# Kernel tuning notes

Hardware: AMD Instinct MI355X
Metric: run time of the kernel (lower is better)

## Reference

```python
import jax, jax.numpy as jnp
import numpy as np

N_NODES = 200000
N_EDGES = 6400000
F_OUT = 128
N_GRAPHS = 64


def setup_inputs() -> dict:
    key = jax.random.key(0)
    ks = jax.random.split(key, 6)
    x = jax.random.normal(ks[0], (N_NODES, 1), dtype=jnp.float32)
    edge_index = jax.random.randint(ks[1], (2, N_EDGES), 0, N_NODES, dtype=jnp.int64)
    batch = jnp.sort(jax.random.randint(ks[2], (N_NODES,), 0, N_GRAPHS, dtype=jnp.int64))
    edge_weights = jax.random.uniform(ks[3], (N_EDGES,), dtype=jnp.float32)
    W_l = jax.random.normal(ks[4], (F_OUT, 1), dtype=jnp.float32)
    b_l = jnp.zeros((F_OUT,), dtype=jnp.float32)
    W_r = jax.random.normal(ks[5], (F_OUT, 1), dtype=jnp.float32)
    return {"x": x, "edge_index": edge_index, "batch": batch,
            "edge_weights": edge_weights, "W_l": W_l, "b_l": b_l, "W_r": W_r}


def reference(x, edge_index, batch, edge_weights, W_l, b_l, W_r):
    # SAGEConv (mean aggregation, edge-weighted messages as in PyG propagate):
    #   out_i = lin_l( mean_{j in N(i)} w_ij * x_j ) + lin_r(x_i)
    n = x.shape[0]
    src, dst = edge_index[0], edge_index[1]
    msgs = x[src] * edge_weights[:, None]                      # [E, 1] gather
    agg_sum = jax.ops.segment_sum(msgs, dst, num_segments=n)  # [N, 1] scatter-add
    deg = jax.ops.segment_sum(jnp.ones((src.shape[0],), x.dtype), dst, num_segments=n)
    agg = agg_sum / jnp.maximum(deg, 1.0)[:, None]             # mean
    h = agg @ W_l.T + b_l + x @ W_r.T                          # [N, F_OUT]
    # dropout(p=0.2) is identity in eval mode -> omitted
    out = jax.ops.segment_max(h, batch, num_segments=N_GRAPHS)  # global_max_pool
    return out
```

## Files before the change

kernel.cpp:

```cpp
#include <hip/hip_runtime.h>
#include <hip/hip_bf16.h>
#include <float.h>
#include <math.h>

constexpr int NN = 200000;
constexpr int NE = 6400000;
constexpr int FO = 128;
constexpr int NG = 64;

constexpr int NCHUNK = 512;
constexpr int CHUNK  = NE / NCHUNK;
constexpr int C4     = CHUNK / 4;
constexpr int BNODES = 1024;
constexpr int NBUK   = (NN + BNODES - 1) / BNODES;

constexpr float Q_SCALE = 4096.0f;
constexpr float Q_INV   = 1.0f / 4096.0f;

__device__ __forceinline__ unsigned encf(float f) {
    unsigned u = __float_as_uint(f);
    return (u & 0x80000000u) ? ~u : (u | 0x80000000u);
}
__device__ __forceinline__ float decf(unsigned e) {
    unsigned u = (e & 0x80000000u) ? (e & 0x7FFFFFFFu) : ~e;
    return __uint_as_float(u);
}

__global__ __launch_bounds__(1024) void k_hist(const int* __restrict__ ei, unsigned* __restrict__ cnt,
                       unsigned* __restrict__ out_enc,
                       const int* __restrict__ batch, int* __restrict__ start) {
    __shared__ unsigned h[NBUK];
    int c = blockIdx.x, tid = threadIdx.x;
    for (int i = tid; i < NBUK; i += 1024) h[i] = 0u;
    if (c == 0) for (int i = tid; i < NG * FO; i += 1024) out_enc[i] = encf(-INFINITY);
    if (c == 1 && tid <= NG) {
        if (tid == NG) start[tid] = NN;
        else {
            int lo = 0, hi = NN;
            while (lo < hi) { int mid = (lo + hi) >> 1; if (batch[mid] < tid) lo = mid + 1; else hi = mid; }
            start[tid] = lo;
        }
    }
    __syncthreads();
    const int4* d4 = (const int4*)(ei + NE + c * CHUNK);
#pragma unroll
    for (int k = 0; k < 4; ++k) {
        int idx = tid + k * 1024;
        if (idx < C4) {
            int4 v = d4[idx];
            atomicAdd(&h[v.x >> 10], 1u);
            atomicAdd(&h[v.y >> 10], 1u);
            atomicAdd(&h[v.z >> 10], 1u);
            atomicAdd(&h[v.w >> 10], 1u);
        }
    }
    __syncthreads();
    for (int i = tid; i < NBUK; i += 1024) cnt[i * NCHUNK + c] = h[i];
}

__global__ void k_scanA(unsigned* __restrict__ cnt, unsigned* __restrict__ T) {
    __shared__ unsigned s[NCHUNK];
    int b = blockIdx.x, t = threadIdx.x;
    unsigned v = cnt[b * NCHUNK + t];
    s[t] = v;
    __syncthreads();
    for (int off = 1; off < NCHUNK; off <<= 1) {
        unsigned u = (t >= off) ? s[t - off] : 0u;
        __syncthreads();
        s[t] += u;
        __syncthreads();
    }
    cnt[b * NCHUNK + t] = s[t] - v;
    if (t == NCHUNK - 1) T[b] = s[t];
}

__global__ void k_scanB(const unsigned* __restrict__ T, unsigned* __restrict__ B) {
    __shared__ unsigned s[256];
    int t = threadIdx.x;
    unsigned v = (t < NBUK) ? T[t] : 0u;
    s[t] = v;
    __syncthreads();
    for (int off = 1; off < 256; off <<= 1) {
        unsigned u = (t >= off) ? s[t - off] : 0u;
        __syncthreads();
        s[t] += u;
        __syncthreads();
    }
    if (t < NBUK) B[t] = s[t] - v;
    if (t == 255) B[NBUK] = s[255];
}

__global__ __launch_bounds__(1024) void k_place(const int* __restrict__ ei, const float* __restrict__ x,
                        const float* __restrict__ w,
                        const unsigned* __restrict__ cnt,
                        const unsigned* __restrict__ T,
                        const unsigned* __restrict__ B,
                        unsigned* __restrict__ rec,
                        int blo, int bhi, unsigned cap) {
    __shared__ unsigned lincl[256];
    __shared__ unsigned loffs[NBUK];
    __shared__ unsigned gbase[NBUK];
    __shared__ unsigned recbuf[CHUNK];
    int c = blockIdx.x, tid = threadIdx.x;
    int nb = bhi - blo;

    unsigned sz = 0;
    if (tid < nb) {
        int b = blo + tid;
        unsigned pre = cnt[b * NCHUNK + c];
        unsigned nxt = (c + 1 < NCHUNK) ? cnt[b * NCHUNK + c + 1] : T[b];
        sz = nxt - pre;
        gbase[b] = B[b] - B[blo] + pre;
    }
    if (tid < 256) lincl[tid] = sz;
    __syncthreads();
    for (int off = 1; off < 256; off <<= 1) {
        unsigned v = 0;
        if (tid < 256 && tid >= off) v = lincl[tid - off];
        __syncthreads();
        if (tid < 256) lincl[tid] += v;
        __syncthreads();
    }
    if (tid < nb) loffs[blo + tid] = lincl[tid] - sz;
    __syncthreads();

    const int4*   s4 = (const int4*)(ei + c * CHUNK);
    const int4*   d4 = (const int4*)(ei + NE + c * CHUNK);
    const float4* w4 = (const float4*)(w + c * CHUNK);
#pragma unroll
    for (int k = 0; k < 4; ++k) {
        int idx = tid + k * 1024;
        if (idx >= C4) continue;
        int4   sv = s4[idx];
        int4   dv = d4[idx];
        float4 wv = w4[idx];
        int    ds[4] = {dv.x, dv.y, dv.z, dv.w};
        int    ss[4] = {sv.x, sv.y, sv.z, sv.w};
        float  wf[4] = {wv.x, wv.y, wv.z, wv.w};
#pragma unroll
        for (int j = 0; j < 4; ++j) {
            int d = ds[j], b = d >> 10;
            if (b < blo || b >= bhi) continue;
            float m = x[ss[j]] * wf[j];
            int q = __float2int_rn(m * Q_SCALE) + 32768;
            q = min(max(q, 0), 65535);
            unsigned lslot = atomicAdd(&loffs[b], 1u);
            recbuf[lslot] = ((unsigned)(d & (BNODES - 1)) << 16) | (unsigned)q;
        }
    }
    __syncthreads();

    int wave = tid >> 6, lane = tid & 63;
    for (int lb = wave; lb < nb; lb += 16) {
        unsigned s0 = lb ? lincl[lb - 1] : 0u;
        unsigned s1 = lincl[lb];
        unsigned g0 = gbase[blo + lb];
        for (unsigned i = s0 + lane; i < s1; i += 64) {
            unsigned g = g0 + (i - s0);
            if (g < cap) rec[g] = recbuf[i];
        }
    }
}

__global__ __launch_bounds__(1024) void k_bucket(const unsigned* __restrict__ rec,
                         const unsigned* __restrict__ B,
                         float* __restrict__ mean, int blo) {
    __shared__ unsigned long long acc[BNODES];
    int b = blo + blockIdx.x, tid = threadIdx.x;
    for (int i = tid; i < BNODES; i += 1024) acc[i] = 0ull;
    __syncthreads();
    unsigned b0 = B[blo];
    unsigned r0 = B[b] - b0, r1 = B[b + 1] - b0;
    for (unsigned r = r0 + tid; r < r1; r += 1024) {
        unsigned v = rec[r];
        atomicAdd(&acc[v >> 16], (1ull << 48) | (unsigned long long)(v & 0xFFFFu));
    }
    __syncthreads();
    int n0 = b * BNODES;
    for (int i = tid; i < BNODES; i += 1024) {
        int n = n0 + i;
        if (n < NN) {
            unsigned long long a = acc[i];
            float cn = (float)(unsigned)(a >> 48);
            float sq = (float)(a & 0xFFFFFFFFFFFFull);
            float sum = (sq - 32768.0f * cn) * Q_INV;
            mean[n] = sum / fmaxf(cn, 1.0f);
        }
    }
}

constexpr int SPLITS = 16;
__global__ void k_max8(const float* __restrict__ mean, const float* __restrict__ x,
                       const float* __restrict__ Wl, const float* __restrict__ Wr,
                       const int* __restrict__ start, unsigned* __restrict__ out_enc) {
    int g = blockIdx.x;
    int lo = start[g], hi = start[g + 1];
    int len = hi - lo;
    if (len <= 0) return;
    int per = (len + gridDim.y - 1) / gridDim.y;
    int a0 = lo + blockIdx.y * per;
    int a1 = min(a0 + per, hi);
    if (a0 >= a1) return;
    int f = threadIdx.x;
    float wl = Wl[f], wr = Wr[f];
    float m0 = -INFINITY, m1 = -INFINITY;
    int i = a0;
    for (; i + 2 <= a1; i += 2) {
        m0 = fmaxf(m0, fmaf(mean[i],     wl, x[i]     * wr));
        m1 = fmaxf(m1, fmaf(mean[i + 1], wl, x[i + 1] * wr));
    }
    if (i < a1) m0 = fmaxf(m0, fmaf(mean[i], wl, x[i] * wr));
    atomicMax(&out_enc[g * FO + f], encf(fmaxf(m0, m1)));
}

__global__ void k_decode(const unsigned* __restrict__ out_enc,
                         const float* __restrict__ bl, float* __restrict__ out) {
    int i = blockIdx.x * blockDim.x + threadIdx.x;
    if (i >= NG * FO) return;
    out[i] = decf(out_enc[i]) + bl[i & (FO - 1)];
}

constexpr float FP_SCALE = 16777216.0f;
constexpr float FP_INV   = 1.0f / FP_SCALE;
__device__ __forceinline__ unsigned long long pack_msg(float m) {
    return (1ull << 48) + (unsigned long long)(__float2ll_rn(m * FP_SCALE) + (1ll << 30));
}
__global__ void k_init1(unsigned long long* __restrict__ agg, unsigned* __restrict__ out_enc,
                        const int* __restrict__ batch, int* __restrict__ start) {
    int i = blockIdx.x * blockDim.x + threadIdx.x;
    if (i < NN) agg[i] = 0ull;
    if (i < NG * FO) out_enc[i] = encf(-INFINITY);
    if (i <= NG) {
        if (i == NG) start[i] = NN;
        else {
            int lo = 0, hi = NN;
            while (lo < hi) { int mid = (lo + hi) >> 1; if (batch[mid] < i) lo = mid + 1; else hi = mid; }
            start[i] = lo;
        }
    }
}
__global__ void k_scatter1(const int* __restrict__ ei, const float* __restrict__ x,
                           const float* __restrict__ w, unsigned long long* __restrict__ agg) {
    int t = blockIdx.x * blockDim.x + threadIdx.x;
    int e0 = t * 4;
    if (e0 >= NE) return;
    int4 sv = *(const int4*)(ei + e0);
    int4 dv = *(const int4*)(ei + NE + e0);
    float4 wv = *(const float4*)(w + e0);
    atomicAdd(&agg[dv.x], pack_msg(x[sv.x] * wv.x));
    atomicAdd(&agg[dv.y], pack_msg(x[sv.y] * wv.y));
    atomicAdd(&agg[dv.z], pack_msg(x[sv.z] * wv.z));
    atomicAdd(&agg[dv.w], pack_msg(x[sv.w] * wv.w));
}
__global__ void k_max1(const unsigned long long* __restrict__ agg, const float* __restrict__ x,
                       const float* __restrict__ Wl, const float* __restrict__ Wr,
                       const int* __restrict__ start, unsigned* __restrict__ out_enc) {
    int g = blockIdx.x;
    int lo = start[g], hi = start[g + 1];
    if (hi - lo <= 0) return;
    int per = (hi - lo + gridDim.y - 1) / gridDim.y;
    int a0 = lo + blockIdx.y * per, a1 = min(a0 + per, hi);
    if (a0 >= a1) return;
    int f = threadIdx.x;
    float wl = Wl[f], wr = Wr[f], m = -INFINITY;
    for (int i = a0; i < a1; ++i) {
        unsigned long long v = agg[i];
        int cnt = (int)(v >> 48);
        long long sfp = (long long)(v & 0xFFFFFFFFFFFFull) - ((long long)cnt << 30);
        float av = ((float)sfp * FP_INV) / fmaxf((float)cnt, 1.0f);
        m = fmaxf(m, fmaf(av, wl, x[i] * wr));
    }
    atomicMax(&out_enc[g * FO + f], encf(m));
}

extern "C" void kernel_launch(void* const* d_in, const int* in_sizes, int n_in,
                              void* d_out, int out_size, void* d_ws, size_t ws_size,
                              hipStream_t stream) {
    const float* x  = (const float*)d_in[0];
    const int*   ei = (const int*)d_in[1];
    const int*   bt = (const int*)d_in[2];
    const float* ew = (const float*)d_in[3];
    const float* Wl = (const float*)d_in[4];
    const float* bl = (const float*)d_in[5];
    const float* Wr = (const float*)d_in[6];
    float* out = (float*)d_out;
    char* ws = (char*)d_ws;

    const size_t FIXED = (size_t)NBUK * NCHUNK * 4
                       + 1024
                       + 1024
                       + 800000
                       + 32768
                       + 512
                       + 256;
    int nphase = 0;
    unsigned cap = 0;
    for (int p = 1; p <= 3; ++p) {
        unsigned c = (unsigned)(NE / p) + 16384u;
        if (ws_size >= FIXED + (size_t)c * 4) { nphase = p; cap = c; break; }
    }

    if (nphase) {
        size_t off = 0;
        unsigned* rec  = (unsigned*)(ws + off); off += (size_t)cap * 4;          off = (off + 15) & ~15ull;
        unsigned* cnt  = (unsigned*)(ws + off); off += (size_t)NBUK * NCHUNK * 4; off = (off + 15) & ~15ull;
        unsigned* T    = (unsigned*)(ws + off); off += 1024;
        unsigned* B    = (unsigned*)(ws + off); off += 1024;
        float*    mean = (float*)(ws + off);    off += 800000;                   off = (off + 15) & ~15ull;
        unsigned* out_enc = (unsigned*)(ws + off); off += 32768;
        int*      start   = (int*)(ws + off);

        k_hist<<<NCHUNK, 1024, 0, stream>>>(ei, cnt, out_enc, bt, start);
        k_scanA<<<NBUK, NCHUNK, 0, stream>>>(cnt, T);
        k_scanB<<<1, 256, 0, stream>>>(T, B);
        int per = (NBUK + nphase - 1) / nphase;
        for (int p = 0; p < nphase; ++p) {
            int blo = p * per;
            int bhi = min(blo + per, NBUK);
            if (blo >= bhi) break;
            k_place<<<NCHUNK, 1024, 0, stream>>>(ei, x, ew, cnt, T, B, rec, blo, bhi, cap);
            k_bucket<<<bhi - blo, 1024, 0, stream>>>(rec, B, mean, blo);
        }
        k_max8<<<dim3(NG, SPLITS), FO, 0, stream>>>(mean, x, Wl, Wr, start, out_enc);
        k_decode<<<(NG * FO + 255) / 256, 256, 0, stream>>>(out_enc, bl, out);
    } else {
        unsigned long long* agg = (unsigned long long*)ws;
        unsigned* out_enc = (unsigned*)(ws + 1600000);
        int*      start   = (int*)(ws + 1600000 + 32768);
        k_init1<<<(NN + 255) / 256, 256, 0, stream>>>(agg, out_enc, bt, start);
        k_scatter1<<<(NE / 4 + 255) / 256, 256, 0, stream>>>(ei, x, ew, agg);
        k_max1<<<dim3(NG, 32), FO, 0, stream>>>(agg, x, Wl, Wr, start, out_enc);
        k_decode<<<(NG * FO + 255) / 256, 256, 0, stream>>>(out_enc, bl, out);
    }
}
```

Before: 84.14 us.

## Compute quantized messages in histogram pass and reuse them in sort

```diff
diff --git a/kernel.cpp b/kernel.cpp
--- a/kernel.cpp
+++ b/kernel.cpp
@@ -26,7 +26,14 @@
     return __uint_as_float(u);
 }
 
-__global__ __launch_bounds__(1024) void k_hist(const int* __restrict__ ei, unsigned* __restrict__ cnt,
+__device__ __forceinline__ unsigned short q16(float m) {
+    int q = __float2int_rn(m * Q_SCALE) + 32768;
+    return (unsigned short)min(max(q, 0), 65535);
+}
+
+__global__ __launch_bounds__(1024) void k_histmsg(const int* __restrict__ ei,
+                       const float* __restrict__ x, const float* __restrict__ w,
+                       unsigned* __restrict__ cnt, unsigned short* __restrict__ msg,
                        unsigned* __restrict__ out_enc,
                        const int* __restrict__ batch, int* __restrict__ start) {
     __shared__ unsigned h[NBUK];
@@ -42,23 +49,33 @@
         }
     }
     __syncthreads();
-    const int4* d4 = (const int4*)(ei + NE + c * CHUNK);
+    const int4*   s4 = (const int4*)(ei + c * CHUNK);
+    const int4*   d4 = (const int4*)(ei + NE + c * CHUNK);
+    const float4* w4 = (const float4*)(w + c * CHUNK);
+    ushort4*      m4 = (ushort4*)(msg + c * CHUNK);
 #pragma unroll
     for (int k = 0; k < 4; ++k) {
         int idx = tid + k * 1024;
-        if (idx < C4) {
-            int4 v = d4[idx];
-            atomicAdd(&h[v.x >> 10], 1u);
-            atomicAdd(&h[v.y >> 10], 1u);
-            atomicAdd(&h[v.z >> 10], 1u);
-            atomicAdd(&h[v.w >> 10], 1u);
-        }
+        if (idx >= C4) continue;
+        int4 dv = d4[idx];
+        atomicAdd(&h[dv.x >> 10], 1u);
+        atomicAdd(&h[dv.y >> 10], 1u);
+        atomicAdd(&h[dv.z >> 10], 1u);
+        atomicAdd(&h[dv.w >> 10], 1u);
+        int4   sv = s4[idx];
+        float4 wv = w4[idx];
+        ushort4 mq;
+        mq.x = q16(x[sv.x] * wv.x);
+        mq.y = q16(x[sv.y] * wv.y);
+        mq.z = q16(x[sv.z] * wv.z);
+        mq.w = q16(x[sv.w] * wv.w);
+        m4[idx] = mq;
     }
     __syncthreads();
     for (int i = tid; i < NBUK; i += 1024) cnt[i * NCHUNK + c] = h[i];
 }
 
-__global__ void k_scanA(unsigned* __restrict__ cnt, unsigned* __restrict__ T) {
+__global__ __launch_bounds__(NCHUNK) void k_scanA(unsigned* __restrict__ cnt, unsigned* __restrict__ T) {
     __shared__ unsigned s[NCHUNK];
     int b = blockIdx.x, t = threadIdx.x;
     unsigned v = cnt[b * NCHUNK + t];
@@ -90,8 +107,8 @@
     if (t == 255) B[NBUK] = s[255];
 }
 
-__global__ __launch_bounds__(1024) void k_place(const int* __restrict__ ei, const float* __restrict__ x,
-                        const float* __restrict__ w,
+__global__ __launch_bounds__(1024) void k_sort(const int* __restrict__ ei,
+                        const unsigned short* __restrict__ msg,
                         const unsigned* __restrict__ cnt,
                         const unsigned* __restrict__ T,
                         const unsigned* __restrict__ B,
@@ -124,28 +141,22 @@
     if (tid < nb) loffs[blo + tid] = lincl[tid] - sz;
     __syncthreads();
 
-    const int4*   s4 = (const int4*)(ei + c * CHUNK);
-    const int4*   d4 = (const int4*)(ei + NE + c * CHUNK);
-    const float4* w4 = (const float4*)(w + c * CHUNK);
+    const int4*    d4 = (const int4*)(ei + NE + c * CHUNK);
+    const ushort4* m4 = (const ushort4*)(msg + c * CHUNK);
 #pragma unroll
     for (int k = 0; k < 4; ++k) {
         int idx = tid + k * 1024;
         if (idx >= C4) continue;
-        int4   sv = s4[idx];
-        int4   dv = d4[idx];
-        float4 wv = w4[idx];
-        int    ds[4] = {dv.x, dv.y, dv.z, dv.w};
-        int    ss[4] = {sv.x, sv.y, sv.z, sv.w};
-        float  wf[4] = {wv.x, wv.y, wv.z, wv.w};
+        int4    dv = d4[idx];
+        ushort4 mv = m4[idx];
+        int      ds_[4] = {dv.x, dv.y, dv.z, dv.w};
+        unsigned mq[4]  = {mv.x, mv.y, mv.z, mv.w};
 #pragma unroll
         for (int j = 0; j < 4; ++j) {
-            int d = ds[j], b = d >> 10;
+            int d = ds_[j], b = d >> 10;
             if (b < blo || b >= bhi) continue;
-            float m = x[ss[j]] * wf[j];
-            int q = __float2int_rn(m * Q_SCALE) + 32768;
-            q = min(max(q, 0), 65535);
-            unsigned lslot = atomicAdd(&loffs[b], 1u);
-            recbuf[lslot] = ((unsigned)(d & (BNODES - 1)) << 16) | (unsigned)q;
+            unsigned ls = atomicAdd(&loffs[b], 1u);
+            recbuf[ls] = ((unsigned)(d & (BNODES - 1)) << 16) | mq[j];
         }
     }
     __syncthreads();
@@ -286,6 +297,7 @@
     float* out = (float*)d_out;
     char* ws = (char*)d_ws;
 
+    const size_t MSG_B = (size_t)NE * 2;
     const size_t FIXED = (size_t)NBUK * NCHUNK * 4
                        + 1024
                        + 1024
@@ -297,20 +309,21 @@
     unsigned cap = 0;
     for (int p = 1; p <= 3; ++p) {
         unsigned c = (unsigned)(NE / p) + 16384u;
-        if (ws_size >= FIXED + (size_t)c * 4) { nphase = p; cap = c; break; }
+        if (ws_size >= FIXED + MSG_B + (size_t)c * 4) { nphase = p; cap = c; break; }
     }
 
     if (nphase) {
         size_t off = 0;
-        unsigned* rec  = (unsigned*)(ws + off); off += (size_t)cap * 4;          off = (off + 15) & ~15ull;
+        unsigned* rec  = (unsigned*)(ws + off); off += (size_t)cap * 4;           off = (off + 15) & ~15ull;
+        unsigned short* msg = (unsigned short*)(ws + off); off += MSG_B;          off = (off + 15) & ~15ull;
         unsigned* cnt  = (unsigned*)(ws + off); off += (size_t)NBUK * NCHUNK * 4; off = (off + 15) & ~15ull;
         unsigned* T    = (unsigned*)(ws + off); off += 1024;
         unsigned* B    = (unsigned*)(ws + off); off += 1024;
-        float*    mean = (float*)(ws + off);    off += 800000;                   off = (off + 15) & ~15ull;
+        float*    mean = (float*)(ws + off);    off += 800000;                    off = (off + 15) & ~15ull;
         unsigned* out_enc = (unsigned*)(ws + off); off += 32768;
         int*      start   = (int*)(ws + off);
 
-        k_hist<<<NCHUNK, 1024, 0, stream>>>(ei, cnt, out_enc, bt, start);
+        k_histmsg<<<NCHUNK, 1024, 0, stream>>>(ei, x, ew, cnt, msg, out_enc, bt, start);
         k_scanA<<<NBUK, NCHUNK, 0, stream>>>(cnt, T);
         k_scanB<<<1, 256, 0, stream>>>(T, B);
         int per = (NBUK + nphase - 1) / nphase;
@@ -318,7 +331,7 @@
             int blo = p * per;
             int bhi = min(blo + per, NBUK);
             if (blo >= bhi) break;
-            k_place<<<NCHUNK, 1024, 0, stream>>>(ei, x, ew, cnt, T, B, rec, blo, bhi, cap);
+            k_sort<<<NCHUNK, 1024, 0, stream>>>(ei, msg, cnt, T, B, rec, blo, bhi, cap);
             k_bucket<<<bhi - blo, 1024, 0, stream>>>(rec, B, mean, blo);
         }
         k_max8<<<dim3(NG, SPLITS), FO, 0, stream>>>(mean, x, Wl, Wr, start, out_enc);
```

After: 82.56 us. No clear change (-1.9%).

## Fuse max-pool into bucket kernel and batch gathers with inline asm in place

Applied to the files above, without the earlier changes.

```diff
diff --git a/kernel.cpp b/kernel.cpp
--- a/kernel.cpp
+++ b/kernel.cpp
@@ -17,6 +17,8 @@
 constexpr float Q_SCALE = 4096.0f;
 constexpr float Q_INV   = 1.0f / 4096.0f;
 
+constexpr unsigned ENC_NINF = 0x007FFFFFu;
+
 __device__ __forceinline__ unsigned encf(float f) {
     unsigned u = __float_as_uint(f);
     return (u & 0x80000000u) ? ~u : (u | 0x80000000u);
@@ -24,6 +26,10 @@
 __device__ __forceinline__ float decf(unsigned e) {
     unsigned u = (e & 0x80000000u) ? (e & 0x7FFFFFFFu) : ~e;
     return __uint_as_float(u);
+}
+__device__ __forceinline__ unsigned short q16(float m) {
+    int q = __float2int_rn(m * Q_SCALE) + 32768;
+    return (unsigned short)min(max(q, 0), 65535);
 }
 
 __global__ __launch_bounds__(1024) void k_hist(const int* __restrict__ ei, unsigned* __restrict__ cnt,
@@ -58,7 +64,7 @@
     for (int i = tid; i < NBUK; i += 1024) cnt[i * NCHUNK + c] = h[i];
 }
 
-__global__ void k_scanA(unsigned* __restrict__ cnt, unsigned* __restrict__ T) {
+__global__ __launch_bounds__(NCHUNK) void k_scanA(unsigned* __restrict__ cnt, unsigned* __restrict__ T) {
     __shared__ unsigned s[NCHUNK];
     int b = blockIdx.x, t = threadIdx.x;
     unsigned v = cnt[b * NCHUNK + t];
@@ -90,8 +96,8 @@
     if (t == 255) B[NBUK] = s[255];
 }
 
-__global__ __launch_bounds__(1024) void k_place(const int* __restrict__ ei, const float* __restrict__ x,
-                        const float* __restrict__ w,
+__global__ __launch_bounds__(1024) void k_sort2(const int* __restrict__ ei,
+                        const float* __restrict__ x, const float* __restrict__ w,
                         const unsigned* __restrict__ cnt,
                         const unsigned* __restrict__ T,
                         const unsigned* __restrict__ B,
@@ -127,90 +133,150 @@
     const int4*   s4 = (const int4*)(ei + c * CHUNK);
     const int4*   d4 = (const int4*)(ei + NE + c * CHUNK);
     const float4* w4 = (const float4*)(w + c * CHUNK);
-#pragma unroll
-    for (int k = 0; k < 4; ++k) {
-        int idx = tid + k * 1024;
-        if (idx >= C4) continue;
-        int4   sv = s4[idx];
-        int4   dv = d4[idx];
-        float4 wv = w4[idx];
-        int    ds[4] = {dv.x, dv.y, dv.z, dv.w};
-        int    ss[4] = {sv.x, sv.y, sv.z, sv.w};
-        float  wf[4] = {wv.x, wv.y, wv.z, wv.w};
-#pragma unroll
-        for (int j = 0; j < 4; ++j) {
-            int d = ds[j], b = d >> 10;
-            if (b < blo || b >= bhi) continue;
-            float m = x[ss[j]] * wf[j];
-            int q = __float2int_rn(m * Q_SCALE) + 32768;
-            q = min(max(q, 0), 65535);
-            unsigned lslot = atomicAdd(&loffs[b], 1u);
-            recbuf[lslot] = ((unsigned)(d & (BNODES - 1)) << 16) | (unsigned)q;
-        }
-    }
+    const bool t3 = tid < (C4 - 3 * 1024);
+
+    int4 dv0 = d4[tid], dv1 = d4[tid + 1024], dv2 = d4[tid + 2048];
+    int4 dv3 = t3 ? d4[tid + 3072] : make_int4(-1, -1, -1, -1);
+    int4 sv0 = s4[tid], sv1 = s4[tid + 1024], sv2 = s4[tid + 2048];
+    int4 sv3 = t3 ? s4[tid + 3072] : make_int4(0, 0, 0, 0);
+    float4 wv0 = w4[tid], wv1 = w4[tid + 1024], wv2 = w4[tid + 2048];
+    float4 wv3 = t3 ? w4[tid + 3072] : make_float4(0.f, 0.f, 0.f, 0.f);
+
+    int bb0 = dv0.x >> 10, bb1 = dv0.y >> 10, bb2  = dv0.z >> 10, bb3  = dv0.w >> 10;
+    int bb4 = dv1.x >> 10, bb5 = dv1.y >> 10, bb6  = dv1.z >> 10, bb7  = dv1.w >> 10;
+    int bb8 = dv2.x >> 10, bb9 = dv2.y >> 10, bb10 = dv2.z >> 10, bb11 = dv2.w >> 10;
+    int bb12 = dv3.x >> 10, bb13 = dv3.y >> 10, bb14 = dv3.z >> 10, bb15 = dv3.w >> 10;
+    unsigned dl0 = (unsigned)(dv0.x & 1023) << 16, dl1 = (unsigned)(dv0.y & 1023) << 16;
+    unsigned dl2 = (unsigned)(dv0.z & 1023) << 16, dl3 = (unsigned)(dv0.w & 1023) << 16;
+    unsigned dl4 = (unsigned)(dv1.x & 1023) << 16, dl5 = (unsigned)(dv1.y & 1023) << 16;
+    unsigned dl6 = (unsigned)(dv1.z & 1023) << 16, dl7 = (unsigned)(dv1.w & 1023) << 16;
+    unsigned dl8 = (unsigned)(dv2.x & 1023) << 16, dl9 = (unsigned)(dv2.y & 1023) << 16;
+    unsigned dl10 = (unsigned)(dv2.z & 1023) << 16, dl11 = (unsigned)(dv2.w & 1023) << 16;
+    unsigned dl12 = (unsigned)(dv3.x & 1023) << 16, dl13 = (unsigned)(dv3.y & 1023) << 16;
+    unsigned dl14 = (unsigned)(dv3.z & 1023) << 16, dl15 = (unsigned)(dv3.w & 1023) << 16;
+    const float *p0 = x + sv0.x, *p1 = x + sv0.y, *p2  = x + sv0.z, *p3  = x + sv0.w;
+    const float *p4 = x + sv1.x, *p5 = x + sv1.y, *p6  = x + sv1.z, *p7  = x + sv1.w;
+    const float *p8 = x + sv2.x, *p9 = x + sv2.y, *p10 = x + sv2.z, *p11 = x + sv2.w;
+    const float *p12 = x + sv3.x, *p13 = x + sv3.y, *p14 = x + sv3.z, *p15 = x + sv3.w;
+
+    float g0, g1, g2, g3, g4, g5, g6, g7, g8, g9, g10, g11, g12, g13, g14, g15;
+    asm volatile(
+        "global_load_dword %0, %8, off\n\t"  "global_load_dword %1, %9, off\n\t"
+        "global_load_dword %2, %10, off\n\t" "global_load_dword %3, %11, off\n\t"
+        "global_load_dword %4, %12, off\n\t" "global_load_dword %5, %13, off\n\t"
+        "global_load_dword %6, %14, off\n\t" "global_load_dword %7, %15, off"
+        : "=&v"(g0), "=&v"(g1), "=&v"(g2), "=&v"(g3),
+          "=&v"(g4), "=&v"(g5), "=&v"(g6), "=&v"(g7)
+        : "v"(p0), "v"(p1), "v"(p2), "v"(p3), "v"(p4), "v"(p5), "v"(p6), "v"(p7));
+    asm volatile(
+        "global_load_dword %0, %8, off\n\t"  "global_load_dword %1, %9, off\n\t"
+        "global_load_dword %2, %10, off\n\t" "global_load_dword %3, %11, off\n\t"
+        "global_load_dword %4, %12, off\n\t" "global_load_dword %5, %13, off\n\t"
+        "global_load_dword %6, %14, off\n\t" "global_load_dword %7, %15, off"
+        : "=&v"(g8), "=&v"(g9), "=&v"(g10), "=&v"(g11),
+          "=&v"(g12), "=&v"(g13), "=&v"(g14), "=&v"(g15)
+        : "v"(p8), "v"(p9), "v"(p10), "v"(p11), "v"(p12), "v"(p13), "v"(p14), "v"(p15));
+
+    unsigned ls0, ls1, ls2, ls3, ls4, ls5, ls6, ls7;
+    unsigned ls8, ls9, ls10, ls11, ls12, ls13, ls14, ls15;
+#define RANK(LS, BB) LS = ((BB) >= blo && (BB) < bhi) ? atomicAdd(&loffs[BB], 1u) : 0xFFFFFFFFu;
+    RANK(ls0, bb0)   RANK(ls1, bb1)   RANK(ls2, bb2)   RANK(ls3, bb3)
+    RANK(ls4, bb4)   RANK(ls5, bb5)   RANK(ls6, bb6)   RANK(ls7, bb7)
+    RANK(ls8, bb8)   RANK(ls9, bb9)   RANK(ls10, bb10) RANK(ls11, bb11)
+    RANK(ls12, bb12) RANK(ls13, bb13) RANK(ls14, bb14) RANK(ls15, bb15)
+#undef RANK
+
+    asm volatile("s_waitcnt vmcnt(0)"
+        : "+v"(g0), "+v"(g1), "+v"(g2), "+v"(g3), "+v"(g4), "+v"(g5), "+v"(g6), "+v"(g7),
+          "+v"(g8), "+v"(g9), "+v"(g10), "+v"(g11), "+v"(g12), "+v"(g13), "+v"(g14), "+v"(g15)
+        :: "memory");
+    __builtin_amdgcn_sched_barrier(0);
+
+#define WREC(LS, DL, G, W) if ((LS) != 0xFFFFFFFFu) recbuf[LS] = (DL) | (unsigned)q16((G) * (W));
+    WREC(ls0, dl0, g0, wv0.x)    WREC(ls1, dl1, g1, wv0.y)
+    WREC(ls2, dl2, g2, wv0.z)    WREC(ls3, dl3, g3, wv0.w)
+    WREC(ls4, dl4, g4, wv1.x)    WREC(ls5, dl5, g5, wv1.y)
+    WREC(ls6, dl6, g6, wv1.z)    WREC(ls7, dl7, g7, wv1.w)
+    WREC(ls8, dl8, g8, wv2.x)    WREC(ls9, dl9, g9, wv2.y)
+    WREC(ls10, dl10, g10, wv2.z) WREC(ls11, dl11, g11, wv2.w)
+    WREC(ls12, dl12, g12, wv3.x) WREC(ls13, dl13, g13, wv3.y)
+    WREC(ls14, dl14, g14, wv3.z) WREC(ls15, dl15, g15, wv3.w)
+#undef WREC
     __syncthreads();
 
     int wave = tid >> 6, lane = tid & 63;
     for (int lb = wave; lb < nb; lb += 16) {
         unsigned s0 = lb ? lincl[lb - 1] : 0u;
         unsigned s1 = lincl[lb];
-        unsigned g0 = gbase[blo + lb];
+        unsigned gb = gbase[blo + lb];
         for (unsigned i = s0 + lane; i < s1; i += 64) {
-            unsigned g = g0 + (i - s0);
+            unsigned g = gb + (i - s0);
             if (g < cap) rec[g] = recbuf[i];
         }
     }
 }
 
-__global__ __launch_bounds__(1024) void k_bucket(const unsigned* __restrict__ rec,
+__global__ __launch_bounds__(1024) void k_bucket2(const unsigned* __restrict__ rec,
                          const unsigned* __restrict__ B,
-                         float* __restrict__ mean, int blo) {
+                         const float* __restrict__ x,
+                         const float* __restrict__ Wl, const float* __restrict__ Wr,
+                         const int* __restrict__ start_g,
+                         unsigned* __restrict__ out_enc, int blo) {
     __shared__ unsigned long long acc[BNODES];
+    __shared__ float2 mx[BNODES];
+    __shared__ unsigned gmax[8 * FO];
+    __shared__ int st[NG + 1];
     int b = blo + blockIdx.x, tid = threadIdx.x;
     for (int i = tid; i < BNODES; i += 1024) acc[i] = 0ull;
-    __syncthreads();
-    unsigned b0 = B[blo];
-    unsigned r0 = B[b] - b0, r1 = B[b + 1] - b0;
+    gmax[tid] = ENC_NINF;
+    if (tid <= NG) st[tid] = start_g[tid];
+    __syncthreads();
+
+    unsigned b0r = B[blo];
+    unsigned r0 = B[b] - b0r, r1 = B[b + 1] - b0r;
     for (unsigned r = r0 + tid; r < r1; r += 1024) {
         unsigned v = rec[r];
         atomicAdd(&acc[v >> 16], (1ull << 48) | (unsigned long long)(v & 0xFFFFu));
     }
     __syncthreads();
+
     int n0 = b * BNODES;
     for (int i = tid; i < BNODES; i += 1024) {
         int n = n0 + i;
-        if (n < NN) {
-            unsigned long long a = acc[i];
-            float cn = (float)(unsigned)(a >> 48);
-            float sq = (float)(a & 0xFFFFFFFFFFFFull);
-            float sum = (sq - 32768.0f * cn) * Q_INV;
-            mean[n] = sum / fmaxf(cn, 1.0f);
-        }
-    }
-}
-
-constexpr int SPLITS = 16;
-__global__ void k_max8(const float* __restrict__ mean, const float* __restrict__ x,
-                       const float* __restrict__ Wl, const float* __restrict__ Wr,
-                       const int* __restrict__ start, unsigned* __restrict__ out_enc) {
-    int g = blockIdx.x;
-    int lo = start[g], hi = start[g + 1];
-    int len = hi - lo;
-    if (len <= 0) return;
-    int per = (len + gridDim.y - 1) / gridDim.y;
-    int a0 = lo + blockIdx.y * per;
-    int a1 = min(a0 + per, hi);
-    if (a0 >= a1) return;
-    int f = threadIdx.x;
+        unsigned long long a = acc[i];
+        float cn = (float)(unsigned)(a >> 48);
+        float sum = ((float)(a & 0xFFFFFFFFFFFFull) - 32768.0f * cn) * Q_INV;
+        mx[i] = make_float2(sum / fmaxf(cn, 1.0f), (n < NN) ? x[n] : 0.f);
+    }
+    __syncthreads();
+
+    int f = tid & (FO - 1);
+    int seg = tid >> 7;
+    int i0 = seg * 128;
     float wl = Wl[f], wr = Wr[f];
-    float m0 = -INFINITY, m1 = -INFINITY;
-    int i = a0;
-    for (; i + 2 <= a1; i += 2) {
-        m0 = fmaxf(m0, fmaf(mean[i],     wl, x[i]     * wr));
-        m1 = fmaxf(m1, fmaf(mean[i + 1], wl, x[i + 1] * wr));
-    }
-    if (i < a1) m0 = fmaxf(m0, fmaf(mean[i], wl, x[i] * wr));
-    atomicMax(&out_enc[g * FO + f], encf(fmaxf(m0, m1)));
+    int g0; { int lo = 0, hi = NG; while (lo < hi) { int m = (lo + hi + 1) >> 1; if (st[m] <= n0) lo = m; else hi = m - 1; } g0 = lo; }
+    int ns = n0 + i0;
+    int g;  { int lo = 0, hi = NG; while (lo < hi) { int m = (lo + hi + 1) >> 1; if (st[m] <= ns) lo = m; else hi = m - 1; } g = lo; }
+    int nxt = (g < NG) ? st[g + 1] : 0x7FFFFFFF;
+    float m = -INFINITY;
+#define FLUSH(G, M) if ((M) > -INFINITY) { int sl = (G) - g0; unsigned ev = encf(M); \
+        if (sl >= 0 && sl < 8) atomicMax(&gmax[sl * FO + f], ev); \
+        else atomicMax(&out_enc[(G) * FO + f], ev); }
+    for (int i = i0; i < i0 + 128; ++i) {
+        int n = n0 + i;
+        if (n >= NN) break;
+        while (n >= nxt) { FLUSH(g, m); m = -INFINITY; ++g; nxt = (g < NG) ? st[g + 1] : 0x7FFFFFFF; }
+        float2 v = mx[i];
+        m = fmaxf(m, fmaf(v.x, wl, v.y * wr));
+    }
+    FLUSH(g, m)
+#undef FLUSH
+    __syncthreads();
+
+    { int s = tid >> 7, ff = tid & (FO - 1);
+      unsigned v = gmax[s * FO + ff];
+      int gg = g0 + s;
+      if (v != ENC_NINF && gg < NG) atomicMax(&out_enc[gg * FO + ff], v); }
 }
 
 __global__ void k_decode(const unsigned* __restrict__ out_enc,
@@ -287,12 +353,9 @@
     char* ws = (char*)d_ws;
 
     const size_t FIXED = (size_t)NBUK * NCHUNK * 4
-                       + 1024
-                       + 1024
-                       + 800000
+                       + 1024 + 1024
                        + 32768
-                       + 512
-                       + 256;
+                       + 512 + 256;
     int nphase = 0;
     unsigned cap = 0;
     for (int p = 1; p <= 3; ++p) {
@@ -302,11 +365,10 @@
 
     if (nphase) {
         size_t off = 0;
-        unsigned* rec  = (unsigned*)(ws + off); off += (size_t)cap * 4;          off = (off + 15) & ~15ull;
+        unsigned* rec  = (unsigned*)(ws + off); off += (size_t)cap * 4;           off = (off + 15) & ~15ull;
         unsigned* cnt  = (unsigned*)(ws + off); off += (size_t)NBUK * NCHUNK * 4; off = (off + 15) & ~15ull;
         unsigned* T    = (unsigned*)(ws + off); off += 1024;
         unsigned* B    = (unsigned*)(ws + off); off += 1024;
-        float*    mean = (float*)(ws + off);    off += 800000;                   off = (off + 15) & ~15ull;
         unsigned* out_enc = (unsigned*)(ws + off); off += 32768;
         int*      start   = (int*)(ws + off);
 
@@ -318,10 +380,9 @@
             int blo = p * per;
             int bhi = min(blo + per, NBUK);
             if (blo >= bhi) break;
-            k_place<<<NCHUNK, 1024, 0, stream>>>(ei, x, ew, cnt, T, B, rec, blo, bhi, cap);
-            k_bucket<<<bhi - blo, 1024, 0, stream>>>(rec, B, mean, blo);
-        }
-        k_max8<<<dim3(NG, SPLITS), FO, 0, stream>>>(mean, x, Wl, Wr, start, out_enc);
+            k_sort2<<<NCHUNK, 1024, 0, stream>>>(ei, x, ew, cnt, T, B, rec, blo, bhi, cap);
+            k_bucket2<<<bhi - blo, 1024, 0, stream>>>(rec, B, x, Wl, Wr, start, out_enc, blo);
+        }
         k_decode<<<(NG * FO + 255) / 256, 256, 0, stream>>>(out_enc, bl, out);
     } else {
         unsigned long long* agg = (unsigned long long*)ws;
```

Result: slower. 95.96 us (+14.0%).
